# Kernel tuning notes

Hardware: AMD Instinct MI355X
Metric: run time of the kernel (lower is better)

The kernel has to match this reference:

```python
import jax, jax.numpy as jnp
import numpy as np

CH = 512
FG = CH // 8  # f/g projection width = 64


def _glorot(key, shape):
    fan_in, fan_out = shape[0], shape[1]
    lim = np.sqrt(6.0 / (fan_in + fan_out))
    return jax.random.uniform(key, shape, jnp.float32, -lim, lim)


def setup_inputs() -> dict:
    key = jax.random.key(0)
    ks = jax.random.split(key, 8)
    B, H, W, C = 4, 64, 64, CH
    return {
        "l": jax.random.normal(ks[0], (B, H, W, C), jnp.float32),
        "r": jax.random.normal(ks[1], (B, H, W, C), jnp.float32),
        # 1x1 conv kernels stored as [C_in, C_out] matrices
        "kernel_f": _glorot(ks[2], (C, FG)),
        "kernel_g": _glorot(ks[3], (C, FG)),
        "kernel_h": _glorot(ks[4], (C, C)),
        "kernel_o": _glorot(ks[5], (C, C)),
        "bias_f": jnp.zeros((FG,), jnp.float32),
        "bias_g": jnp.zeros((FG,), jnp.float32),
        "bias_h": jnp.zeros((C,), jnp.float32),
        # original code (buggily) glorot-inits bias_o; replicate a nonzero init
        "bias_o": jax.random.uniform(ks[6], (C,), jnp.float32, -0.05, 0.05),
    }


def _proj(x, w, b):
    # 1x1 conv + bias + relu: [B,H,W,Cin] @ [Cin,Cout]
    return jax.nn.relu(jnp.einsum("bhwc,cd->bhwd", x, w) + b)


def reference(l, r, kernel_f, kernel_g, kernel_h, kernel_o,
              bias_f, bias_g, bias_h, bias_o):
    B, H, W, C = l.shape
    N = H * W
    g = _proj(r, kernel_g, bias_g).reshape(B, N, FG)   # queries from r
    f = _proj(l, kernel_f, bias_f).reshape(B, N, FG)   # keys from l
    h = _proj(l, kernel_h, bias_h).reshape(B, N, C)    # values from l
    # unscaled attention scores [B, N, N]
    s = jnp.einsum("bnd,bmd->bnm", g, f)
    beta = jax.nn.softmax(s, axis=-1)
    o = jnp.einsum("bnm,bmc->bnc", beta, h).reshape(B, H, W, C)
    o = _proj(o, kernel_o, bias_o)
    return o, beta
```

## Files before the change

kernel.cpp:

```cpp
#include <hip/hip_runtime.h>
#include <hip/hip_bf16.h>


#define BATCH 4
#define NSEQ  4096
#define CHN   512
#define FGW   64
#define MROWS (BATCH * NSEQ)

using f32x4  = __attribute__((ext_vector_type(4))) float;
using bf16x8 = __attribute__((ext_vector_type(8))) short;
using u32x4  = __attribute__((ext_vector_type(4))) unsigned int;

__device__ __forceinline__ unsigned short f2bf(float f) {
  union { __hip_bfloat16 h; unsigned short u; } v;
  v.h = __float2bfloat16(f);
  return v.u;
}
__device__ __forceinline__ float bf2f(unsigned short u) {
  return __uint_as_float(((unsigned int)u) << 16);
}
__device__ __forceinline__ int swz(int r, int c) {
  return r * 64 + (c ^ ((r & 7) << 3));
}
__device__ __forceinline__ bf16x8 ld8(const unsigned short* base, int r, int c) {
  return *reinterpret_cast<const bf16x8*>(base + swz(r, c));
}

__global__ __launch_bounds__(256) void cast_bf16_kernel(
    const float* __restrict__ in, unsigned short* __restrict__ out) {
  int i = (blockIdx.x * 256 + threadIdx.x) * 4;
  float4 v = *reinterpret_cast<const float4*>(in + i);
  ushort4 o;
  o.x = f2bf(v.x); o.y = f2bf(v.y); o.z = f2bf(v.z); o.w = f2bf(v.w);
  *reinterpret_cast<ushort4*>(out + i) = o;
}

__global__ __launch_bounds__(256) void transpose_w_kernel(
    const float* __restrict__ w, unsigned short* __restrict__ wt) {
  int t = blockIdx.x * 256 + threadIdx.x;
  int k = t >> 9, n = t & 511;
  wt[n * 512 + k] = f2bf(w[t]);
}

__global__ __launch_bounds__(256) void fg_proj_kernel(
    const float* __restrict__ x, const float* __restrict__ w,
    const float* __restrict__ bias,
    unsigned short* __restrict__ out_hi, unsigned short* __restrict__ out_lo) {
  __shared__ float xs[16][512];
  const int t = threadIdx.x;
  const int row0 = blockIdx.x * 16;
  {
    const float4* src = reinterpret_cast<const float4*>(x + (size_t)row0 * 512);
    float4* dst = reinterpret_cast<float4*>(&xs[0][0]);
#pragma unroll
    for (int i = 0; i < 8; i++) dst[t + i * 256] = src[t + i * 256];
  }
  __syncthreads();
  const int col = t & 63;
  const int rb = (t >> 6) * 4;
  float a0 = 0.f, a1 = 0.f, a2 = 0.f, a3 = 0.f;
#pragma unroll 8
  for (int k = 0; k < 512; k++) {
    float wv = w[k * 64 + col];
    a0 = fmaf(xs[rb + 0][k], wv, a0);
    a1 = fmaf(xs[rb + 1][k], wv, a1);
    a2 = fmaf(xs[rb + 2][k], wv, a2);
    a3 = fmaf(xs[rb + 3][k], wv, a3);
  }
  const float bv = bias[col];
  float av[4] = {a0, a1, a2, a3};
#pragma unroll
  for (int j = 0; j < 4; j++) {
    float v = fmaxf(av[j] + bv, 0.f);
    unsigned short hi = f2bf(v);
    unsigned short lo = f2bf(v - bf2f(hi));
    size_t idx = (size_t)(row0 + rb + j) * FGW + col;
    out_hi[idx] = hi;
    out_lo[idx] = lo;
  }
}

template <int MODE>
__global__ __launch_bounds__(256) void gemm512_kernel(
    const unsigned short* __restrict__ A,
    const unsigned short* __restrict__ Bt,
    const float* __restrict__ bias,
    void* __restrict__ outp) {
  __shared__ unsigned short As[128 * 64], Bs[128 * 64];
  const int t = threadIdx.x;
  const int lane = t & 63;
  const int wid = t >> 6;
  const int wr = wid >> 1, wc = wid & 1;
  const int m0 = blockIdx.y * 128;
  const int n0 = blockIdx.x * 128;

  f32x4 acc[4][4] = {};
  const int srow = t >> 1;
  const int spart = (t & 1) * 32;
#pragma unroll 1
  for (int kt = 0; kt < 8; kt++) {
    const int k0 = kt * 64;
    __syncthreads();
    {
      const unsigned short* ga = A + (size_t)(m0 + srow) * 512 + k0 + spart;
      const unsigned short* gb = Bt + (size_t)(n0 + srow) * 512 + k0 + spart;
#pragma unroll
      for (int i = 0; i < 4; i++) {
        u32x4 va = *reinterpret_cast<const u32x4*>(ga + i * 8);
        u32x4 vb = *reinterpret_cast<const u32x4*>(gb + i * 8);
        *reinterpret_cast<u32x4*>(As + swz(srow, spart + i * 8)) = va;
        *reinterpret_cast<u32x4*>(Bs + swz(srow, spart + i * 8)) = vb;
      }
    }
    __syncthreads();
#pragma unroll
    for (int ks = 0; ks < 2; ks++) {
      const int koff = ks * 32 + (lane >> 4) * 8;
      bf16x8 a[4], bb[4];
#pragma unroll
      for (int rt = 0; rt < 4; rt++) a[rt] = ld8(As, wr * 64 + rt * 16 + (lane & 15), koff);
#pragma unroll
      for (int ct = 0; ct < 4; ct++) bb[ct] = ld8(Bs, wc * 64 + ct * 16 + (lane & 15), koff);
#pragma unroll
      for (int rt = 0; rt < 4; rt++)
#pragma unroll
        for (int ct = 0; ct < 4; ct++)
          acc[rt][ct] = __builtin_amdgcn_mfma_f32_16x16x32_bf16(a[rt], bb[ct], acc[rt][ct], 0, 0, 0);
    }
  }
#pragma unroll
  for (int rt = 0; rt < 4; rt++)
#pragma unroll
    for (int ct = 0; ct < 4; ct++) {
      const int n = n0 + wc * 64 + ct * 16 + (lane & 15);
      const float bv = bias[n];
      const int rowb = m0 + wr * 64 + rt * 16 + (lane >> 4) * 4;
      if (MODE == 0) {
        unsigned short* ht = (unsigned short*)outp;
        const int bb2 = rowb >> 12, key = rowb & 4095;
        ushort4 v;
        v.x = f2bf(fmaxf(acc[rt][ct][0] + bv, 0.f));
        v.y = f2bf(fmaxf(acc[rt][ct][1] + bv, 0.f));
        v.z = f2bf(fmaxf(acc[rt][ct][2] + bv, 0.f));
        v.w = f2bf(fmaxf(acc[rt][ct][3] + bv, 0.f));
        *reinterpret_cast<ushort4*>(ht + ((size_t)bb2 * CHN + n) * NSEQ + key) = v;
      } else {
        float* oo = (float*)outp;
#pragma unroll
        for (int rr = 0; rr < 4; rr++)
          oo[(size_t)(rowb + rr) * CHN + n] = fmaxf(acc[rt][ct][rr] + bv, 0.f);
      }
    }
}

__global__ __launch_bounds__(256) void attn_kernel(
    const unsigned short* __restrict__ g_hi, const unsigned short* __restrict__ g_lo,
    const unsigned short* __restrict__ f_hi, const unsigned short* __restrict__ f_lo,
    const unsigned short* __restrict__ h_t,
    float* __restrict__ beta_out,
    unsigned short* __restrict__ o_att) {
  __shared__ unsigned short gs_hi[32 * 64], gs_lo[32 * 64];
  __shared__ unsigned short fs_hi[64 * 64], fs_lo[64 * 64];
  __shared__ float p_f32[32][68];
  __shared__ unsigned short p_bf[32 * 64];
  __shared__ float m_sc[4][32], l_sc[4][32];

  const int t = threadIdx.x;
  const int lane = t & 63;
  const int w = t >> 6;
  const int bid = blockIdx.x;
  const int b = bid >> 7;
  const int q0 = (bid & 127) << 5;
  const size_t gqrow = (size_t)b * NSEQ + q0;

  {
    const u32x4* shi = reinterpret_cast<const u32x4*>(g_hi + gqrow * FGW);
    const u32x4* slo = reinterpret_cast<const u32x4*>(g_lo + gqrow * FGW);
    int row = t >> 3, c8 = (t & 7) * 8;
    int di = swz(row, c8) >> 3;
    reinterpret_cast<u32x4*>(gs_hi)[di] = shi[t];
    reinterpret_cast<u32x4*>(gs_lo)[di] = slo[t];
  }
  __syncthreads();

  bf16x8 ag_hi[2][2], ag_lo[2][2];
#pragma unroll
  for (int rt = 0; rt < 2; rt++)
#pragma unroll
    for (int ks = 0; ks < 2; ks++) {
      int koff = ks * 32 + (lane >> 4) * 8;
      ag_hi[rt][ks] = ld8(gs_hi, rt * 16 + (lane & 15), koff);
      ag_lo[rt][ks] = ld8(gs_lo, rt * 16 + (lane & 15), koff);
    }

  float m_run[2][4], l_run[2][4];
#pragma unroll
  for (int rt = 0; rt < 2; rt++)
#pragma unroll
    for (int r = 0; r < 4; r++) { m_run[rt][r] = -INFINITY; l_run[rt][r] = 0.f; }

  for (int kb = 0; kb < 64; kb++) {
    __syncthreads();
    {
      const size_t fbase = ((size_t)b * NSEQ + kb * 64) * FGW;
      const u32x4* shi = reinterpret_cast<const u32x4*>(f_hi + fbase);
      const u32x4* slo = reinterpret_cast<const u32x4*>(f_lo + fbase);
      u32x4* dhi = reinterpret_cast<u32x4*>(fs_hi);
      u32x4* dlo = reinterpret_cast<u32x4*>(fs_lo);
#pragma unroll
      for (int i = 0; i < 2; i++) {
        int cid = t + i * 256;
        int row = cid >> 3, c8 = (cid & 7) * 8;
        int di = swz(row, c8) >> 3;
        dhi[di] = shi[cid];
        dlo[di] = slo[cid];
      }
    }
    __syncthreads();

    f32x4 sacc[2] = {};
#pragma unroll
    for (int ks = 0; ks < 2; ks++) {
      int koff = ks * 32 + (lane >> 4) * 8;
      bf16x8 bh = ld8(fs_hi, w * 16 + (lane & 15), koff);
      bf16x8 bl = ld8(fs_lo, w * 16 + (lane & 15), koff);
#pragma unroll
      for (int rt = 0; rt < 2; rt++) {
        sacc[rt] = __builtin_amdgcn_mfma_f32_16x16x32_bf16(ag_hi[rt][ks], bh, sacc[rt], 0, 0, 0);
        sacc[rt] = __builtin_amdgcn_mfma_f32_16x16x32_bf16(ag_hi[rt][ks], bl, sacc[rt], 0, 0, 0);
        sacc[rt] = __builtin_amdgcn_mfma_f32_16x16x32_bf16(ag_lo[rt][ks], bh, sacc[rt], 0, 0, 0);
      }
    }
#pragma unroll
    for (int rt = 0; rt < 2; rt++)
#pragma unroll
      for (int r = 0; r < 4; r++) {
        float s = sacc[rt][r];
        float mx = s;
        mx = fmaxf(mx, __shfl_xor(mx, 1));
        mx = fmaxf(mx, __shfl_xor(mx, 2));
        mx = fmaxf(mx, __shfl_xor(mx, 4));
        mx = fmaxf(mx, __shfl_xor(mx, 8));
        float mn = fmaxf(m_run[rt][r], mx);
        float e = __expf(s - mn);
        e += __shfl_xor(e, 1);
        e += __shfl_xor(e, 2);
        e += __shfl_xor(e, 4);
        e += __shfl_xor(e, 8);
        l_run[rt][r] = l_run[rt][r] * __expf(m_run[rt][r] - mn) + e;
        m_run[rt][r] = mn;
      }
  }

  if ((lane & 15) == 0) {
#pragma unroll
    for (int rt = 0; rt < 2; rt++)
#pragma unroll
      for (int r = 0; r < 4; r++) {
        int row = rt * 16 + (lane >> 4) * 4 + r;
        m_sc[w][row] = m_run[rt][r];
        l_sc[w][row] = l_run[rt][r];
      }
  }
  __syncthreads();
  float m_fin[2][4], li_fin[2][4];
#pragma unroll
  for (int rt = 0; rt < 2; rt++)
#pragma unroll
    for (int r = 0; r < 4; r++) {
      int row = rt * 16 + (lane >> 4) * 4 + r;
      float mf = m_sc[0][row];
      for (int w2 = 1; w2 < 4; w2++) mf = fmaxf(mf, m_sc[w2][row]);
      float lf = 0.f;
      for (int w2 = 0; w2 < 4; w2++) lf += l_sc[w2][row] * __expf(m_sc[w2][row] - mf);
      m_fin[rt][r] = mf;
      li_fin[rt][r] = 1.f / lf;
    }

  f32x4 oacc[2][8] = {};
  for (int kb = 0; kb < 64; kb++) {
    __syncthreads();
    {
      const size_t fbase = ((size_t)b * NSEQ + kb * 64) * FGW;
      const u32x4* shi = reinterpret_cast<const u32x4*>(f_hi + fbase);
      const u32x4* slo = reinterpret_cast<const u32x4*>(f_lo + fbase);
      u32x4* dhi = reinterpret_cast<u32x4*>(fs_hi);
      u32x4* dlo = reinterpret_cast<u32x4*>(fs_lo);
#pragma unroll
      for (int i = 0; i < 2; i++) {
        int cid = t + i * 256;
        int row = cid >> 3, c8 = (cid & 7) * 8;
        int di = swz(row, c8) >> 3;
        dhi[di] = shi[cid];
        dlo[di] = slo[cid];
      }
    }
    __syncthreads();

    f32x4 sacc[2] = {};
#pragma unroll
    for (int ks = 0; ks < 2; ks++) {
      int koff = ks * 32 + (lane >> 4) * 8;
      bf16x8 bh = ld8(fs_hi, w * 16 + (lane & 15), koff);
      bf16x8 bl = ld8(fs_lo, w * 16 + (lane & 15), koff);
#pragma unroll
      for (int rt = 0; rt < 2; rt++) {
        sacc[rt] = __builtin_amdgcn_mfma_f32_16x16x32_bf16(ag_hi[rt][ks], bh, sacc[rt], 0, 0, 0);
        sacc[rt] = __builtin_amdgcn_mfma_f32_16x16x32_bf16(ag_hi[rt][ks], bl, sacc[rt], 0, 0, 0);
        sacc[rt] = __builtin_amdgcn_mfma_f32_16x16x32_bf16(ag_lo[rt][ks], bh, sacc[rt], 0, 0, 0);
      }
    }
#pragma unroll
    for (int rt = 0; rt < 2; rt++)
#pragma unroll
      for (int r = 0; r < 4; r++) {
        float bta = __expf(sacc[rt][r] - m_fin[rt][r]) * li_fin[rt][r];
        int row = rt * 16 + (lane >> 4) * 4 + r;
        int ck = w * 16 + (lane & 15);
        p_f32[row][ck] = bta;
        p_bf[swz(row, ck)] = f2bf(bta);
      }
    __syncthreads();

    {
      int row = t >> 3, c = (t & 7) * 8;
      float* dst = beta_out + ((size_t)(b * NSEQ + q0 + row)) * NSEQ + kb * 64 + c;
      const float* srcp = &p_f32[row][c];
      *reinterpret_cast<float4*>(dst) = *reinterpret_cast<const float4*>(srcp);
      *reinterpret_cast<float4*>(dst + 4) = *reinterpret_cast<const float4*>(srcp + 4);
    }

#pragma unroll
    for (int ks = 0; ks < 2; ks++) {
      int koff = ks * 32 + (lane >> 4) * 8;
      bf16x8 ap0 = ld8(p_bf, (lane & 15), koff);
      bf16x8 ap1 = ld8(p_bf, 16 + (lane & 15), koff);
#pragma unroll
      for (int ct = 0; ct < 8; ct++) {
        int col = w * 128 + ct * 16 + (lane & 15);
        bf16x8 bh = *reinterpret_cast<const bf16x8*>(
            h_t + ((size_t)b * CHN + col) * NSEQ + kb * 64 + koff);
        oacc[0][ct] = __builtin_amdgcn_mfma_f32_16x16x32_bf16(ap0, bh, oacc[0][ct], 0, 0, 0);
        oacc[1][ct] = __builtin_amdgcn_mfma_f32_16x16x32_bf16(ap1, bh, oacc[1][ct], 0, 0, 0);
      }
    }
  }

#pragma unroll
  for (int rt = 0; rt < 2; rt++)
#pragma unroll
    for (int ct = 0; ct < 8; ct++) {
      int col = w * 128 + ct * 16 + (lane & 15);
#pragma unroll
      for (int r = 0; r < 4; r++) {
        int row = rt * 16 + (lane >> 4) * 4 + r;
        o_att[((size_t)(b * NSEQ + q0 + row)) * CHN + col] = f2bf(oacc[rt][ct][r]);
      }
    }
}

extern "C" void kernel_launch(void* const* d_in, const int* in_sizes, int n_in,
                              void* d_out, int out_size, void* d_ws, size_t ws_size,
                              hipStream_t stream) {
  (void)in_sizes; (void)n_in; (void)out_size; (void)ws_size;
  const float* l   = (const float*)d_in[0];
  const float* r   = (const float*)d_in[1];
  const float* wf  = (const float*)d_in[2];
  const float* wg  = (const float*)d_in[3];
  const float* wh  = (const float*)d_in[4];
  const float* wo  = (const float*)d_in[5];
  const float* bf_ = (const float*)d_in[6];
  const float* bg  = (const float*)d_in[7];
  const float* bh  = (const float*)d_in[8];
  const float* bo  = (const float*)d_in[9];

  char* ws = (char*)d_ws;
  unsigned short* f_hi  = (unsigned short*)(ws + (0ull  << 20));
  unsigned short* f_lo  = (unsigned short*)(ws + (2ull  << 20));
  unsigned short* g_hi  = (unsigned short*)(ws + (4ull  << 20));
  unsigned short* g_lo  = (unsigned short*)(ws + (6ull  << 20));
  unsigned short* l_bf  = (unsigned short*)(ws + (8ull  << 20));
  unsigned short* wh_t  = (unsigned short*)(ws + (24ull << 20));
  unsigned short* wo_t  = (unsigned short*)(ws + (25ull << 20));
  unsigned short* h_t   = (unsigned short*)(ws + (26ull << 20));
  unsigned short* o_att = (unsigned short*)(ws + (42ull << 20));

  float* out_o = (float*)d_out;
  float* out_beta = out_o + (size_t)MROWS * CHN;

  cast_bf16_kernel<<<MROWS * CHN / 1024, 256, 0, stream>>>(l, l_bf);
  transpose_w_kernel<<<512 * 512 / 256, 256, 0, stream>>>(wh, wh_t);
  transpose_w_kernel<<<512 * 512 / 256, 256, 0, stream>>>(wo, wo_t);
  fg_proj_kernel<<<MROWS / 16, 256, 0, stream>>>(l, wf, bf_, f_hi, f_lo);
  fg_proj_kernel<<<MROWS / 16, 256, 0, stream>>>(r, wg, bg, g_hi, g_lo);
  gemm512_kernel<0><<<dim3(4, 128), 256, 0, stream>>>(l_bf, wh_t, bh, (void*)h_t);
  attn_kernel<<<512, 256, 0, stream>>>(g_hi, g_lo, f_hi, f_lo, h_t, out_beta, o_att);
  gemm512_kernel<1><<<dim3(4, 128), 256, 0, stream>>>(o_att, wo_t, bo, (void*)out_o);
}
```

Measured before the change: 1.105 ms.

## Split attention into split-K stats pass, merge, and 16-row output kernel

Moves the softmax max/sum pass out of the fused attention kernel into a separate stats kernel that splits the key dimension into 8 chunks for many more blocks, followed by a merge kernel. The main attention kernel now uses 16-row query tiles (1024 blocks), loads f directly into registers with prefetching instead of staging through LDS, double-buffers the probability tile so each iteration needs one barrier, and remaps blocks across XCDs. It aims to raise occupancy and parallelism and cut synchronisation, but it reads h twice as often per query, issues uncoalesced per-lane beta stores, and adds two extra kernel launches.

```diff
diff --git a/kernel.cpp b/kernel.cpp
--- a/kernel.cpp
+++ b/kernel.cpp
@@ -7,6 +7,8 @@
 #define CHN   512
 #define FGW   64
 #define MROWS (BATCH * NSEQ)
+#define KCH   8
+#define KCHLEN (NSEQ / KCH)
 
 using f32x4  = __attribute__((ext_vector_type(4))) float;
 using bf16x8 = __attribute__((ext_vector_type(8))) short;
@@ -154,210 +156,189 @@
     }
 }
 
-__global__ __launch_bounds__(256) void attn_kernel(
+__global__ __launch_bounds__(256) void stats_kernel(
+    const unsigned short* __restrict__ g_hi, const unsigned short* __restrict__ g_lo,
+    const unsigned short* __restrict__ f_hi, const unsigned short* __restrict__ f_lo,
+    float2* __restrict__ mpart) {
+  __shared__ float msc[4][16], lsc[4][16];
+  const int t = threadIdx.x, lane = t & 63, w = t >> 6;
+  const int bid = blockIdx.x;
+  const int kc = bid & 7;
+  const int qt = (bid >> 3) & 255;
+  const int b = bid >> 11;
+  const size_t grow = (size_t)b * NSEQ + qt * 16;
+  const int koff = (lane >> 4) * 8;
+
+  bf16x8 agh[2], agl[2];
+  {
+    const unsigned short* gh = g_hi + (grow + (lane & 15)) * FGW;
+    const unsigned short* gl = g_lo + (grow + (lane & 15)) * FGW;
+#pragma unroll
+    for (int ks = 0; ks < 2; ks++) {
+      agh[ks] = *reinterpret_cast<const bf16x8*>(gh + ks * 32 + koff);
+      agl[ks] = *reinterpret_cast<const bf16x8*>(gl + ks * 32 + koff);
+    }
+  }
+  float m_run[4], l_run[4];
+#pragma unroll
+  for (int r = 0; r < 4; r++) { m_run[r] = -INFINITY; l_run[r] = 0.f; }
+
+  const size_t frow = (size_t)b * NSEQ + kc * KCHLEN + w * 16 + (lane & 15);
+#pragma unroll 1
+  for (int kb = 0; kb < KCHLEN / 64; kb++) {
+    const unsigned short* fh = f_hi + (frow + kb * 64) * FGW;
+    const unsigned short* fl = f_lo + (frow + kb * 64) * FGW;
+    f32x4 sacc = {};
+#pragma unroll
+    for (int ks = 0; ks < 2; ks++) {
+      bf16x8 bh = *reinterpret_cast<const bf16x8*>(fh + ks * 32 + koff);
+      bf16x8 bl = *reinterpret_cast<const bf16x8*>(fl + ks * 32 + koff);
+      sacc = __builtin_amdgcn_mfma_f32_16x16x32_bf16(agh[ks], bh, sacc, 0, 0, 0);
+      sacc = __builtin_amdgcn_mfma_f32_16x16x32_bf16(agh[ks], bl, sacc, 0, 0, 0);
+      sacc = __builtin_amdgcn_mfma_f32_16x16x32_bf16(agl[ks], bh, sacc, 0, 0, 0);
+    }
+#pragma unroll
+    for (int r = 0; r < 4; r++) {
+      float s = sacc[r];
+      float mx = s;
+      mx = fmaxf(mx, __shfl_xor(mx, 1));
+      mx = fmaxf(mx, __shfl_xor(mx, 2));
+      mx = fmaxf(mx, __shfl_xor(mx, 4));
+      mx = fmaxf(mx, __shfl_xor(mx, 8));
+      float mn = fmaxf(m_run[r], mx);
+      float e = __expf(s - mn);
+      e += __shfl_xor(e, 1);
+      e += __shfl_xor(e, 2);
+      e += __shfl_xor(e, 4);
+      e += __shfl_xor(e, 8);
+      l_run[r] = l_run[r] * __expf(m_run[r] - mn) + e;
+      m_run[r] = mn;
+    }
+  }
+  if ((lane & 15) == 0) {
+#pragma unroll
+    for (int r = 0; r < 4; r++) {
+      int row = (lane >> 4) * 4 + r;
+      msc[w][row] = m_run[r];
+      lsc[w][row] = l_run[r];
+    }
+  }
+  __syncthreads();
+  if (w == 0 && lane < 16) {
+    float m = msc[0][lane];
+    for (int w2 = 1; w2 < 4; w2++) m = fmaxf(m, msc[w2][lane]);
+    float l = 0.f;
+    for (int w2 = 0; w2 < 4; w2++) l += lsc[w2][lane] * __expf(msc[w2][lane] - m);
+    mpart[(grow + lane) * KCH + kc] = make_float2(m, l);
+  }
+}
+
+__global__ __launch_bounds__(256) void stats_merge_kernel(
+    const float2* __restrict__ mpart, float* __restrict__ m_fin,
+    float* __restrict__ li_fin) {
+  int row = blockIdx.x * 256 + threadIdx.x;
+  float2 v[KCH];
+#pragma unroll
+  for (int i = 0; i < KCH; i++) v[i] = mpart[(size_t)row * KCH + i];
+  float m = v[0].x;
+#pragma unroll
+  for (int i = 1; i < KCH; i++) m = fmaxf(m, v[i].x);
+  float l = 0.f;
+#pragma unroll
+  for (int i = 0; i < KCH; i++) l += v[i].y * __expf(v[i].x - m);
+  m_fin[row] = m;
+  li_fin[row] = 1.f / l;
+}
+
+__global__ __launch_bounds__(256, 3) void attn2_kernel(
     const unsigned short* __restrict__ g_hi, const unsigned short* __restrict__ g_lo,
     const unsigned short* __restrict__ f_hi, const unsigned short* __restrict__ f_lo,
     const unsigned short* __restrict__ h_t,
-    float* __restrict__ beta_out,
-    unsigned short* __restrict__ o_att) {
-  __shared__ unsigned short gs_hi[32 * 64], gs_lo[32 * 64];
-  __shared__ unsigned short fs_hi[64 * 64], fs_lo[64 * 64];
-  __shared__ float p_f32[32][68];
-  __shared__ unsigned short p_bf[32 * 64];
-  __shared__ float m_sc[4][32], l_sc[4][32];
-
-  const int t = threadIdx.x;
-  const int lane = t & 63;
-  const int w = t >> 6;
+    const float* __restrict__ m_fin, const float* __restrict__ li_fin,
+    float* __restrict__ beta_out, unsigned short* __restrict__ o_att) {
+  __shared__ unsigned short p_bf[2][16 * 64];
+  const int t = threadIdx.x, lane = t & 63, w = t >> 6;
   const int bid = blockIdx.x;
-  const int b = bid >> 7;
-  const int q0 = (bid & 127) << 5;
-  const size_t gqrow = (size_t)b * NSEQ + q0;
-
+  const int xcd = bid & 7, j = bid >> 3;
+  const int b = xcd & 3;
+  const int qt = (xcd >> 2) * 128 + j;
+  const size_t grow = (size_t)b * NSEQ + qt * 16;
+  const int koff = (lane >> 4) * 8;
+  const int rbase = (lane >> 4) * 4;
+
+  bf16x8 agh[2], agl[2];
   {
-    const u32x4* shi = reinterpret_cast<const u32x4*>(g_hi + gqrow * FGW);
-    const u32x4* slo = reinterpret_cast<const u32x4*>(g_lo + gqrow * FGW);
-    int row = t >> 3, c8 = (t & 7) * 8;
-    int di = swz(row, c8) >> 3;
-    reinterpret_cast<u32x4*>(gs_hi)[di] = shi[t];
-    reinterpret_cast<u32x4*>(gs_lo)[di] = slo[t];
-  }
-  __syncthreads();
-
-  bf16x8 ag_hi[2][2], ag_lo[2][2];
-#pragma unroll
-  for (int rt = 0; rt < 2; rt++)
-#pragma unroll
-    for (int ks = 0; ks < 2; ks++) {
-      int koff = ks * 32 + (lane >> 4) * 8;
-      ag_hi[rt][ks] = ld8(gs_hi, rt * 16 + (lane & 15), koff);
-      ag_lo[rt][ks] = ld8(gs_lo, rt * 16 + (lane & 15), koff);
-    }
-
-  float m_run[2][4], l_run[2][4];
-#pragma unroll
-  for (int rt = 0; rt < 2; rt++)
-#pragma unroll
-    for (int r = 0; r < 4; r++) { m_run[rt][r] = -INFINITY; l_run[rt][r] = 0.f; }
-
+    const unsigned short* gh = g_hi + (grow + (lane & 15)) * FGW;
+    const unsigned short* gl = g_lo + (grow + (lane & 15)) * FGW;
+#pragma unroll
+    for (int ks = 0; ks < 2; ks++) {
+      agh[ks] = *reinterpret_cast<const bf16x8*>(gh + ks * 32 + koff);
+      agl[ks] = *reinterpret_cast<const bf16x8*>(gl + ks * 32 + koff);
+    }
+  }
+  float m_r[4], li_r[4];
+#pragma unroll
+  for (int r = 0; r < 4; r++) {
+    m_r[r] = m_fin[grow + rbase + r];
+    li_r[r] = li_fin[grow + rbase + r];
+  }
+
+  const unsigned short* fb_h = f_hi + ((size_t)b * NSEQ + w * 16 + (lane & 15)) * FGW;
+  const unsigned short* fb_l = f_lo + ((size_t)b * NSEQ + w * 16 + (lane & 15)) * FGW;
+  bf16x8 fh[2], fl[2];
+#pragma unroll
+  for (int ks = 0; ks < 2; ks++) {
+    fh[ks] = *reinterpret_cast<const bf16x8*>(fb_h + ks * 32 + koff);
+    fl[ks] = *reinterpret_cast<const bf16x8*>(fb_l + ks * 32 + koff);
+  }
+
+  const unsigned short* hb = h_t + ((size_t)b * CHN + w * 128 + (lane & 15)) * NSEQ;
+  f32x4 oacc[8] = {};
+
+#pragma unroll 1
   for (int kb = 0; kb < 64; kb++) {
+    f32x4 sacc = {};
+#pragma unroll
+    for (int ks = 0; ks < 2; ks++) {
+      sacc = __builtin_amdgcn_mfma_f32_16x16x32_bf16(agh[ks], fh[ks], sacc, 0, 0, 0);
+      sacc = __builtin_amdgcn_mfma_f32_16x16x32_bf16(agh[ks], fl[ks], sacc, 0, 0, 0);
+      sacc = __builtin_amdgcn_mfma_f32_16x16x32_bf16(agl[ks], fh[ks], sacc, 0, 0, 0);
+    }
+    const int buf = kb & 1;
+#pragma unroll
+    for (int r = 0; r < 4; r++) {
+      float bta = __expf(sacc[r] - m_r[r]) * li_r[r];
+      beta_out[(grow + rbase + r) * (size_t)NSEQ + kb * 64 + w * 16 + (lane & 15)] = bta;
+      p_bf[buf][swz(rbase + r, w * 16 + (lane & 15))] = f2bf(bta);
+    }
     __syncthreads();
-    {
-      const size_t fbase = ((size_t)b * NSEQ + kb * 64) * FGW;
-      const u32x4* shi = reinterpret_cast<const u32x4*>(f_hi + fbase);
-      const u32x4* slo = reinterpret_cast<const u32x4*>(f_lo + fbase);
-      u32x4* dhi = reinterpret_cast<u32x4*>(fs_hi);
-      u32x4* dlo = reinterpret_cast<u32x4*>(fs_lo);
-#pragma unroll
-      for (int i = 0; i < 2; i++) {
-        int cid = t + i * 256;
-        int row = cid >> 3, c8 = (cid & 7) * 8;
-        int di = swz(row, c8) >> 3;
-        dhi[di] = shi[cid];
-        dlo[di] = slo[cid];
+    if (kb < 63) {
+      const unsigned short* nh = fb_h + (size_t)(kb + 1) * 64 * FGW;
+      const unsigned short* nl = fb_l + (size_t)(kb + 1) * 64 * FGW;
+#pragma unroll
+      for (int ks = 0; ks < 2; ks++) {
+        fh[ks] = *reinterpret_cast<const bf16x8*>(nh + ks * 32 + koff);
+        fl[ks] = *reinterpret_cast<const bf16x8*>(nl + ks * 32 + koff);
       }
     }
-    __syncthreads();
-
-    f32x4 sacc[2] = {};
-#pragma unroll
-    for (int ks = 0; ks < 2; ks++) {
-      int koff = ks * 32 + (lane >> 4) * 8;
-      bf16x8 bh = ld8(fs_hi, w * 16 + (lane & 15), koff);
-      bf16x8 bl = ld8(fs_lo, w * 16 + (lane & 15), koff);
-#pragma unroll
-      for (int rt = 0; rt < 2; rt++) {
-        sacc[rt] = __builtin_amdgcn_mfma_f32_16x16x32_bf16(ag_hi[rt][ks], bh, sacc[rt], 0, 0, 0);
-        sacc[rt] = __builtin_amdgcn_mfma_f32_16x16x32_bf16(ag_hi[rt][ks], bl, sacc[rt], 0, 0, 0);
-        sacc[rt] = __builtin_amdgcn_mfma_f32_16x16x32_bf16(ag_lo[rt][ks], bh, sacc[rt], 0, 0, 0);
+    const unsigned short* hkb = hb + kb * 64 + koff;
+#pragma unroll
+    for (int ks = 0; ks < 2; ks++) {
+      bf16x8 ap = ld8(p_bf[buf], lane & 15, ks * 32 + koff);
+#pragma unroll
+      for (int ct = 0; ct < 8; ct++) {
+        bf16x8 hv = *reinterpret_cast<const bf16x8*>(hkb + (size_t)ct * 16 * NSEQ + ks * 32);
+        oacc[ct] = __builtin_amdgcn_mfma_f32_16x16x32_bf16(ap, hv, oacc[ct], 0, 0, 0);
       }
     }
-#pragma unroll
-    for (int rt = 0; rt < 2; rt++)
-#pragma unroll
-      for (int r = 0; r < 4; r++) {
-        float s = sacc[rt][r];
-        float mx = s;
-        mx = fmaxf(mx, __shfl_xor(mx, 1));
-        mx = fmaxf(mx, __shfl_xor(mx, 2));
-        mx = fmaxf(mx, __shfl_xor(mx, 4));
-        mx = fmaxf(mx, __shfl_xor(mx, 8));
-        float mn = fmaxf(m_run[rt][r], mx);
-        float e = __expf(s - mn);
-        e += __shfl_xor(e, 1);
-        e += __shfl_xor(e, 2);
-        e += __shfl_xor(e, 4);
-        e += __shfl_xor(e, 8);
-        l_run[rt][r] = l_run[rt][r] * __expf(m_run[rt][r] - mn) + e;
-        m_run[rt][r] = mn;
-      }
-  }
-
-  if ((lane & 15) == 0) {
-#pragma unroll
-    for (int rt = 0; rt < 2; rt++)
-#pragma unroll
-      for (int r = 0; r < 4; r++) {
-        int row = rt * 16 + (lane >> 4) * 4 + r;
-        m_sc[w][row] = m_run[rt][r];
-        l_sc[w][row] = l_run[rt][r];
-      }
-  }
-  __syncthreads();
-  float m_fin[2][4], li_fin[2][4];
-#pragma unroll
-  for (int rt = 0; rt < 2; rt++)
-#pragma unroll
-    for (int r = 0; r < 4; r++) {
-      int row = rt * 16 + (lane >> 4) * 4 + r;
-      float mf = m_sc[0][row];
-      for (int w2 = 1; w2 < 4; w2++) mf = fmaxf(mf, m_sc[w2][row]);
-      float lf = 0.f;
-      for (int w2 = 0; w2 < 4; w2++) lf += l_sc[w2][row] * __expf(m_sc[w2][row] - mf);
-      m_fin[rt][r] = mf;
-      li_fin[rt][r] = 1.f / lf;
-    }
-
-  f32x4 oacc[2][8] = {};
-  for (int kb = 0; kb < 64; kb++) {
-    __syncthreads();
-    {
-      const size_t fbase = ((size_t)b * NSEQ + kb * 64) * FGW;
-      const u32x4* shi = reinterpret_cast<const u32x4*>(f_hi + fbase);
-      const u32x4* slo = reinterpret_cast<const u32x4*>(f_lo + fbase);
-      u32x4* dhi = reinterpret_cast<u32x4*>(fs_hi);
-      u32x4* dlo = reinterpret_cast<u32x4*>(fs_lo);
-#pragma unroll
-      for (int i = 0; i < 2; i++) {
-        int cid = t + i * 256;
-        int row = cid >> 3, c8 = (cid & 7) * 8;
-        int di = swz(row, c8) >> 3;
-        dhi[di] = shi[cid];
-        dlo[di] = slo[cid];
-      }
-    }
-    __syncthreads();
-
-    f32x4 sacc[2] = {};
-#pragma unroll
-    for (int ks = 0; ks < 2; ks++) {
-      int koff = ks * 32 + (lane >> 4) * 8;
-      bf16x8 bh = ld8(fs_hi, w * 16 + (lane & 15), koff);
-      bf16x8 bl = ld8(fs_lo, w * 16 + (lane & 15), koff);
-#pragma unroll
-      for (int rt = 0; rt < 2; rt++) {
-        sacc[rt] = __builtin_amdgcn_mfma_f32_16x16x32_bf16(ag_hi[rt][ks], bh, sacc[rt], 0, 0, 0);
-        sacc[rt] = __builtin_amdgcn_mfma_f32_16x16x32_bf16(ag_hi[rt][ks], bl, sacc[rt], 0, 0, 0);
-        sacc[rt] = __builtin_amdgcn_mfma_f32_16x16x32_bf16(ag_lo[rt][ks], bh, sacc[rt], 0, 0, 0);
-      }
-    }
-#pragma unroll
-    for (int rt = 0; rt < 2; rt++)
-#pragma unroll
-      for (int r = 0; r < 4; r++) {
-        float bta = __expf(sacc[rt][r] - m_fin[rt][r]) * li_fin[rt][r];
-        int row = rt * 16 + (lane >> 4) * 4 + r;
-        int ck = w * 16 + (lane & 15);
-        p_f32[row][ck] = bta;
-        p_bf[swz(row, ck)] = f2bf(bta);
-      }
-    __syncthreads();
-
-    {
-      int row = t >> 3, c = (t & 7) * 8;
-      float* dst = beta_out + ((size_t)(b * NSEQ + q0 + row)) * NSEQ + kb * 64 + c;
-      const float* srcp = &p_f32[row][c];
-      *reinterpret_cast<float4*>(dst) = *reinterpret_cast<const float4*>(srcp);
-      *reinterpret_cast<float4*>(dst + 4) = *reinterpret_cast<const float4*>(srcp + 4);
-    }
-
-#pragma unroll
-    for (int ks = 0; ks < 2; ks++) {
-      int koff = ks * 32 + (lane >> 4) * 8;
-      bf16x8 ap0 = ld8(p_bf, (lane & 15), koff);
-      bf16x8 ap1 = ld8(p_bf, 16 + (lane & 15), koff);
-#pragma unroll
-      for (int ct = 0; ct < 8; ct++) {
-        int col = w * 128 + ct * 16 + (lane & 15);
-        bf16x8 bh = *reinterpret_cast<const bf16x8*>(
-            h_t + ((size_t)b * CHN + col) * NSEQ + kb * 64 + koff);
-        oacc[0][ct] = __builtin_amdgcn_mfma_f32_16x16x32_bf16(ap0, bh, oacc[0][ct], 0, 0, 0);
-        oacc[1][ct] = __builtin_amdgcn_mfma_f32_16x16x32_bf16(ap1, bh, oacc[1][ct], 0, 0, 0);
-      }
-    }
-  }
-
-#pragma unroll
-  for (int rt = 0; rt < 2; rt++)
-#pragma unroll
-    for (int ct = 0; ct < 8; ct++) {
-      int col = w * 128 + ct * 16 + (lane & 15);
-#pragma unroll
-      for (int r = 0; r < 4; r++) {
-        int row = rt * 16 + (lane >> 4) * 4 + r;
-        o_att[((size_t)(b * NSEQ + q0 + row)) * CHN + col] = f2bf(oacc[rt][ct][r]);
-      }
-    }
+  }
+#pragma unroll
+  for (int ct = 0; ct < 8; ct++) {
+    int col = w * 128 + ct * 16 + (lane & 15);
+#pragma unroll
+    for (int r = 0; r < 4; r++)
+      o_att[(grow + rbase + r) * CHN + col] = f2bf(oacc[ct][r]);
+  }
 }
 
 extern "C" void kernel_launch(void* const* d_in, const int* in_sizes, int n_in,
@@ -385,6 +366,9 @@
   unsigned short* wo_t  = (unsigned short*)(ws + (25ull << 20));
   unsigned short* h_t   = (unsigned short*)(ws + (26ull << 20));
   unsigned short* o_att = (unsigned short*)(ws + (42ull << 20));
+  float2*         mpart = (float2*)(ws + (58ull << 20));
+  float*          m_fin = (float*)(ws + (59ull << 20));
+  float*          li_fin= (float*)(ws + (59ull << 20) + (1ull << 19));
 
   float* out_o = (float*)d_out;
   float* out_beta = out_o + (size_t)MROWS * CHN;
@@ -395,6 +379,9 @@
   fg_proj_kernel<<<MROWS / 16, 256, 0, stream>>>(l, wf, bf_, f_hi, f_lo);
   fg_proj_kernel<<<MROWS / 16, 256, 0, stream>>>(r, wg, bg, g_hi, g_lo);
   gemm512_kernel<0><<<dim3(4, 128), 256, 0, stream>>>(l_bf, wh_t, bh, (void*)h_t);
-  attn_kernel<<<512, 256, 0, stream>>>(g_hi, g_lo, f_hi, f_lo, h_t, out_beta, o_att);
+  stats_kernel<<<BATCH * 256 * KCH, 256, 0, stream>>>(g_hi, g_lo, f_hi, f_lo, mpart);
+  stats_merge_kernel<<<MROWS / 256, 256, 0, stream>>>(mpart, m_fin, li_fin);
+  attn2_kernel<<<1024, 256, 0, stream>>>(g_hi, g_lo, f_hi, f_lo, h_t, m_fin, li_fin,
+                                         out_beta, o_att);
   gemm512_kernel<1><<<dim3(4, 128), 256, 0, stream>>>(o_att, wo_t, bo, (void*)out_o);
 }
```

Result: slower. 1.139 ms (+3.1%).
